# Kernel optimization log

Hardware: AMD Instinct MI355X
Metric: run time of the kernel (lower is better)

Reference implementation:

```python
import jax, jax.numpy as jnp
import numpy as np

K = 16          # max_points
S = 3           # num_scales
DM = 256        # d_model
KD = 16         # k_dim geometric projection
TAU = 1e-4
LN_EPS = 1e-5


def _boundaries():
    edges = [(i, j) for i in range(K) for j in range(i + 1, K)]
    tris = [(i, j, k) for i in range(K) for j in range(i + 1, K) for k in range(j + 1, K)]
    E, T = len(edges), len(tris)
    B1 = np.zeros((K, E), np.float32)
    for e, (i, j) in enumerate(edges):
        B1[i, e] = -1.0
        B1[j, e] = 1.0
    eidx = {e: n for n, e in enumerate(edges)}
    B2 = np.zeros((E, T), np.float32)
    for t, (i, j, k) in enumerate(tris):
        B2[eidx[(j, k)], t] = 1.0
        B2[eidx[(i, k)], t] = -1.0
        B2[eidx[(i, j)], t] = 1.0
    ei = np.array([e[0] for e in edges])
    ej = np.array([e[1] for e in edges])
    tij = np.array([eidx[(a, b)] for a, b, c in tris])
    tjk = np.array([eidx[(b, c)] for a, b, c in tris])
    tik = np.array([eidx[(a, c)] for a, b, c in tris])
    return (jnp.asarray(B1), jnp.asarray(B2), jnp.asarray(np.abs(B1)),
            jnp.asarray(ei), jnp.asarray(ej), jnp.asarray(tij), jnp.asarray(tjk), jnp.asarray(tik))

_B1, _B2, _ABS, _EI, _EJ, _TIJ, _TJK, _TIK = _boundaries()
E = _B1.shape[1]  # 120


def _ln(x, g, b):
    m = jnp.mean(x, -1, keepdims=True)
    v = jnp.mean((x - m) ** 2, -1, keepdims=True)
    return (x - m) * jax.lax.rsqrt(v + LN_EPS) * g + b


def setup_inputs() -> dict:
    key = jax.random.key(0)
    ks = jax.random.split(key, 12)
    B = 1024
    p = lambda k, *sh: 0.02 * jax.random.normal(k, sh, dtype=jnp.float32)
    return {
        'x': jax.random.normal(ks[0], (B, K, DM), dtype=jnp.float32),
        'mask': jnp.ones((B, K), dtype=jnp.float32),
        'Wg': p(ks[1], DM, KD), 'bg': jnp.zeros((KD,), jnp.float32),
        'log_scales': jnp.linspace(-1.5, 1.5, S, dtype=jnp.float32),
        'Wv': p(ks[2], DM, DM * S), 'bv': jnp.zeros((DM * S,), jnp.float32),
        'We': p(ks[3], DM, DM * S), 'be': jnp.zeros((DM * S,), jnp.float32),
        'Wo': p(ks[4], DM * S * 2, DM), 'bo': jnp.zeros((DM,), jnp.float32),
        'ln1_g': jnp.ones((DM,), jnp.float32), 'ln1_b': jnp.zeros((DM,), jnp.float32),
        'ln2_g': jnp.ones((DM,), jnp.float32), 'ln2_b': jnp.zeros((DM,), jnp.float32),
        'Wf1': p(ks[5], DM, DM * 4), 'bf1': jnp.zeros((DM * 4,), jnp.float32),
        'Wf2': p(ks[6], DM * 4, DM), 'bf2': jnp.zeros((DM,), jnp.float32),
    }


def reference(x, mask, Wg, bg, log_scales, Wv, bv, We, be, Wo, bo,
              ln1_g, ln1_b, ln2_g, ln2_b, Wf1, bf1, Wf2, bf2):
    B = x.shape[0]
    xn = _ln(x, ln1_g, ln1_b)
    P = xn @ Wg + bg                                   # [B,K,KD]
    m2 = mask[:, :, None] * mask[:, None, :]           # [B,K,K]
    p2 = jnp.sum(P * P, -1)
    Dsq = jnp.maximum(p2[:, :, None] + p2[:, None, :] - 2.0 * jnp.einsum('bkc,blc->bkl', P, P), 0.0) * m2
    sig2 = jnp.exp(log_scales) ** 2                    # [S]
    V0 = (xn @ Wv + bv).reshape(B, K, S, DM).transpose(0, 2, 1, 3)   # [B,S,K,D]
    Eraw = jnp.einsum('ke,bkd->bed', _ABS, xn)         # [B,E,D]
    Ein = (Eraw @ We + be).reshape(B, E, S, DM).transpose(0, 2, 1, 3)  # [B,S,E,D]
    aff = jnp.exp(-Dsq[:, None] / (2.0 * sig2[None, :, None, None] + 1e-8)) * m2[:, None]  # [B,S,K,K]
    W1 = aff[:, :, _EI, _EJ]                           # [B,S,E]
    W2 = W1[:, :, _TIJ] * W1[:, :, _TJK] * W1[:, :, _TIK]  # [B,S,T]
    L0 = jnp.einsum('ke,bse,le->bskl', _B1, W1, _B1) + TAU * jnp.eye(K, dtype=x.dtype)
    node_upd = jnp.einsum('bskl,bsld->bskd', L0, V0)
    term_down = jnp.einsum('ke,bk,kf->bef', _B1, mask, _B1)
    term_up = jnp.einsum('et,bst,ft->bsef', _B2, W2, _B2)
    L1 = term_down[:, None] + term_up + TAU * jnp.eye(E, dtype=x.dtype)
    edge_msg = jnp.einsum('bsef,bsfd->bsed', L1, Ein)
    edge_upd = jnp.einsum('ke,bsed->bskd', _ABS, edge_msg)
    nu = node_upd.transpose(0, 2, 1, 3).reshape(B, K, S * DM)
    eu = edge_upd.transpose(0, 2, 1, 3).reshape(B, K, S * DM)
    x = x + (jnp.concatenate([nu, eu], -1) @ Wo + bo)  # residual + attn_out (dropout=eval noop)
    h = _ln(x, ln2_g, ln2_b)
    return x + (jax.nn.gelu(h @ Wf1 + bf1, approximate=False) @ Wf2 + bf2)
```

## Files before the change

### kernel.cpp

```cpp
#include <hip/hip_runtime.h>
#include <hip/hip_bf16.h>
#include <cstdint>
#include <cstddef>

#define TAU 1e-4f
#define LN_EPS 1e-5f

typedef unsigned short ushort_t;
typedef unsigned int uint_t;
typedef __attribute__((ext_vector_type(8))) short short8;
typedef __attribute__((ext_vector_type(4))) float f32x4;

__device__ __forceinline__ ushort_t f2bf(float f) {
    union { float f; unsigned int u; } c; c.f = f;
    unsigned int r = (c.u + 0x7fffu + ((c.u >> 16) & 1u)) >> 16;
    return (ushort_t)r;
}
__device__ __forceinline__ void glds16(const void* g, void* l) {
    __builtin_amdgcn_global_load_lds((const __attribute__((address_space(1))) unsigned int*)g,
                                     (__attribute__((address_space(3))) unsigned int*)l,
                                     16, 0, 0);
}

__global__ __launch_bounds__(256) void kA(
    const float* __restrict__ xg, const float* __restrict__ maskg,
    const float* __restrict__ Wg, const float* __restrict__ bg,
    const float* __restrict__ ls, const float* __restrict__ g1,
    const float* __restrict__ b1, ushort_t* __restrict__ Mcat,
    float* __restrict__ gbuf,
    const float* __restrict__ Wv, const float* __restrict__ We,
    const float* __restrict__ Wo, const float* __restrict__ bv,
    const float* __restrict__ be, const float* __restrict__ Wf1,
    const float* __restrict__ Wf2, ushort_t* __restrict__ WcatT,
    ushort_t* __restrict__ Wf1T, ushort_t* __restrict__ Wf2T,
    float* __restrict__ cvpart, float* __restrict__ beWo) {
    __shared__ __align__(16) float POOL[9872];
    const int tid = threadIdx.x;

    if (blockIdx.x >= 1024) {
        const int id = blockIdx.x - 1024;
        if (id < 384) {
            float (*rowS)[256] = (float(*)[256])POOL;
            const int q0 = (id & 63) * 4;
            const int w = id >> 6;
            const int half = w / 3, s = w - half * 3;
            const float* src = half ? We : Wv;
#pragma unroll
            for (int r = 0; r < 4; ++r)
                rowS[r][tid] = src[(size_t)(q0 + r) * 768 + s * 256 + tid];
            __syncthreads();
            const float* wo = Wo + (size_t)(half * 768 + s * 256) * 256 + tid;
            float a0 = 0.f, a1 = 0.f, a2 = 0.f, a3 = 0.f;
            for (int d = 0; d < 256; ++d) {
                float wv = wo[(size_t)d * 256];
                a0 += rowS[0][d] * wv; a1 += rowS[1][d] * wv;
                a2 += rowS[2][d] * wv; a3 += rowS[3][d] * wv;
            }
            const int rt = half * 3 + s;
            ushort4 pk;
            pk.x = f2bf(a0); pk.y = f2bf(a1); pk.z = f2bf(a2); pk.w = f2bf(a3);
            *(ushort4*)&WcatT[(size_t)tid * 1536 + rt * 256 + q0] = pk;
        } else if (id < 390) {
            const int w = id - 384;
            const int half = w / 3, s = w - half * 3;
            const float* vec = half ? be : bv;
            POOL[tid] = vec[s * 256 + tid];
            __syncthreads();
            const float* wo = Wo + (size_t)(half * 768 + s * 256) * 256 + tid;
            float acc = 0.f;
            for (int d = 0; d < 256; ++d) acc += POOL[d] * wo[(size_t)d * 256];
            if (half) beWo[s * 256 + tid] = acc;
            else cvpart[s * 256 + tid] = acc;
        } else {
            float (*tS)[65] = (float(*)[65])POOL;
            const float* src; ushort_t* dst;
            int sr0, sc0, ss, dr0, dc0, ds_;
            if (id < 454) {
                int t = id - 390; int ki = t & 3, ni = t >> 2;
                src = Wf1; ss = 1024; sr0 = ki * 64; sc0 = ni * 64;
                dst = Wf1T; ds_ = 256; dr0 = ni * 64; dc0 = ki * 64;
            } else {
                int t = id - 454; int ki = t >> 2, ni = t & 3;
                src = Wf2; ss = 256; sr0 = ki * 64; sc0 = ni * 64;
                dst = Wf2T; ds_ = 1024; dr0 = ni * 64; dc0 = ki * 64;
            }
            const int rl = tid >> 6, cl = tid & 63;
#pragma unroll
            for (int p = 0; p < 16; ++p) {
                int r = p * 4 + rl;
                tS[r][cl] = src[(size_t)(sr0 + r) * ss + sc0 + cl];
            }
            __syncthreads();
#pragma unroll
            for (int p = 0; p < 16; ++p) {
                int r = p * 4 + rl;
                dst[(size_t)(dr0 + r) * ds_ + dc0 + cl] = f2bf(tS[cl][r]);
            }
        }
        return;
    }

    const int b = blockIdx.x;
    float (*XS)[260] = (float(*)[260])POOL;
    float* WB = POOL + 4160;
    float (*Pl)[17] = (float(*)[17])(POOL + 8320);
    float (*dotm)[17] = (float(*)[17])(POOL + 8592);
    float* Ms = POOL + 8320;
    float* mk = POOL + 9856;
    float (*WgT)[260] = (float(*)[260])WB;
    float (*DsqS)[17] = (float(*)[17])WB;
    float (*Wh)[16][17] = (float(*)[16][17])(WB + 272);
    float* Ts = WB + 1088;

    const float* xb = xg + (size_t)b * 4096;
#pragma unroll
    for (int i = 0; i < 4; ++i) {
        int idx = tid * 4 + i * 1024;
        int k = idx >> 8, c = idx & 255;
        float4 v = *(const float4*)&xb[idx];
        XS[k][c] = v.x; XS[k][c + 1] = v.y; XS[k][c + 2] = v.z; XS[k][c + 3] = v.w;
    }
    {
        const float4* wgp = (const float4*)(Wg + tid * 16);
        float4 w0 = wgp[0], w1 = wgp[1], w2 = wgp[2], w3 = wgp[3];
        WgT[0][tid] = w0.x; WgT[1][tid] = w0.y; WgT[2][tid] = w0.z; WgT[3][tid] = w0.w;
        WgT[4][tid] = w1.x; WgT[5][tid] = w1.y; WgT[6][tid] = w1.z; WgT[7][tid] = w1.w;
        WgT[8][tid] = w2.x; WgT[9][tid] = w2.y; WgT[10][tid] = w2.z; WgT[11][tid] = w2.w;
        WgT[12][tid] = w3.x; WgT[13][tid] = w3.y; WgT[14][tid] = w3.z; WgT[15][tid] = w3.w;
    }
    if (tid < 16) mk[tid] = maskg[b * 16 + tid];
    __syncthreads();

    {
        const int k = tid >> 4, c = tid & 15;
        float s = 0.f;
#pragma unroll
        for (int j = 0; j < 16; ++j) s += XS[k][c + 16 * j];
        for (int off = 8; off; off >>= 1) s += __shfl_down(s, off, 16);
        float mean = __shfl(s, 0, 16) * (1.f / 256.f);
        float vs = 0.f;
#pragma unroll
        for (int j = 0; j < 16; ++j) { float d = XS[k][c + 16 * j] - mean; vs += d * d; }
        for (int off = 8; off; off >>= 1) vs += __shfl_down(vs, off, 16);
        float rstd = rsqrtf(__shfl(vs, 0, 16) * (1.f / 256.f) + LN_EPS);
#pragma unroll
        for (int j = 0; j < 16; ++j) {
            int cc = c + 16 * j;
            XS[k][cc] = (XS[k][cc] - mean) * rstd * g1[cc] + b1[cc];
        }
    }
    __syncthreads();

    {
        const int k = tid >> 4, c = tid & 15;
        float acc = bg[c];
#pragma unroll
        for (int q4 = 0; q4 < 64; ++q4) {
            float4 wv = *(const float4*)&WgT[c][q4 * 4];
            float4 xv = *(const float4*)&XS[k][q4 * 4];
            acc += wv.x * xv.x + wv.y * xv.y + wv.z * xv.z + wv.w * xv.w;
        }
        Pl[k][c] = acc;
    }
    __syncthreads();
    const int k = tid >> 4, m = tid & 15;
    {
        float d = 0.f;
#pragma unroll
        for (int c = 0; c < 16; ++c) d += Pl[k][c] * Pl[m][c];
        dotm[k][m] = d;
    }
    __syncthreads();
    {
        float v = dotm[k][k] + dotm[m][m] - 2.f * dotm[k][m];
        DsqS[k][m] = fmaxf(v, 0.f) * mk[k] * mk[m];
    }
    {
        float d = DsqS[k][m];
        float mm = mk[k] * mk[m];
#pragma unroll
        for (int s = 0; s < 3; ++s) {
            float i2 = 1.f / (2.f * expf(2.f * ls[s]) + 1e-8f);
            Wh[s][k][m] = (k == m) ? 0.f : expf(-d * i2) * mm;
        }
    }
    __syncthreads();
    if (tid < 48) {
        int s = tid >> 4, j = tid & 15;
        float t = 0.f;
        for (int i = 0; i < j; ++i) {
            float d = 0.f;
            for (int jj = j + 1; jj < 16; ++jj) d += Wh[s][j][jj] * Wh[s][i][jj];
            t += Wh[s][i][j] * d;
        }
        Ts[s * 16 + j] = t;
    }
    __syncthreads();
    float gd = 0.f;
#pragma unroll
    for (int o = 0; o < 16; ++o) {
        if (o == m) continue;
        int u = o < m ? o : m, v = o < m ? m : o;
        float gu = (u == k) ? (float)(2 * k - 15) : ((u > k) ? 1.f : -1.f);
        float gv = (v == k) ? (float)(2 * k - 15) : ((v > k) ? 1.f : -1.f);
        gd += -gu * mk[u] + gv * mk[v];
        if (u == k || v == k) gd += TAU;
    }
#pragma unroll
    for (int s = 0; s < 3; ++s) {
        float rs = 0.f;
#pragma unroll
        for (int o = 0; o < 16; ++o) rs += Wh[s][k][o];
        float l0 = (k == m) ? (rs + TAU) : -Wh[s][k][m];
        float G = gd + ((k == m) ? 4.f * Ts[s * 16 + k] : 0.f);
        Ms[s * 256 + tid] = l0;
        Ms[768 + s * 256 + tid] = G;
        float gg = G;
        for (int off = 8; off; off >>= 1) gg += __shfl_down(gg, off, 16);
        if (m == 0) gbuf[b * 48 + k * 3 + s] = 0.5f * gg;
    }
    __syncthreads();

    {
        const int q2 = (tid & 127) * 2;
        const int rtbase = (tid >> 7) * 3;
        float xv0[16], xv1[16];
#pragma unroll
        for (int l = 0; l < 16; ++l) { xv0[l] = XS[l][q2]; xv1[l] = XS[l][q2 + 1]; }
        const size_t obase = (size_t)b * 16 * 1536;
#pragma unroll
        for (int rtt = 0; rtt < 3; ++rtt) {
            const int rt = rtbase + rtt;
#pragma unroll
            for (int kk = 0; kk < 16; ++kk) {
                const float4* mp = (const float4*)&Ms[rt * 256 + kk * 16];
                float4 m0 = mp[0], m1 = mp[1], m2 = mp[2], m3 = mp[3];
                float a0 = m0.x * xv0[0] + m0.y * xv0[1] + m0.z * xv0[2] + m0.w * xv0[3]
                         + m1.x * xv0[4] + m1.y * xv0[5] + m1.z * xv0[6] + m1.w * xv0[7]
                         + m2.x * xv0[8] + m2.y * xv0[9] + m2.z * xv0[10] + m2.w * xv0[11]
                         + m3.x * xv0[12] + m3.y * xv0[13] + m3.z * xv0[14] + m3.w * xv0[15];
                float a1 = m0.x * xv1[0] + m0.y * xv1[1] + m0.z * xv1[2] + m0.w * xv1[3]
                         + m1.x * xv1[4] + m1.y * xv1[5] + m1.z * xv1[6] + m1.w * xv1[7]
                         + m2.x * xv1[8] + m2.y * xv1[9] + m2.z * xv1[10] + m2.w * xv1[11]
                         + m3.x * xv1[12] + m3.y * xv1[13] + m3.z * xv1[14] + m3.w * xv1[15];
                uint_t pk = (uint_t)f2bf(a0) | ((uint_t)f2bf(a1) << 16);
                *(uint_t*)&Mcat[obase + (size_t)kk * 1536 + rt * 256 + q2] = pk;
            }
        }
    }
}

__device__ __forceinline__ void gemm64_db(
    const ushort_t* __restrict__ A, const ushort_t* __restrict__ Bt,
    int Kdim, int m0, int n0, f32x4 acc[2][4],
    ushort_t (*As0)[32], ushort_t (*As1)[32],
    ushort_t (*Bs0)[32], ushort_t (*Bs1)[32]) {
    const int tid = threadIdx.x;
    const int wave = tid >> 6, lane = tid & 63;
    const int lq = lane >> 4, lr = lane & 15;
    const int wm = wave >> 1, wn = wave & 1;
    const int r = tid >> 2, ca = (tid & 3) << 3;
    const ushort_t* Ag  = A  + (size_t)(m0 + r) * Kdim + ca;
    const ushort_t* Bg0 = Bt + (size_t)(n0 + r) * Kdim + ca;
    const ushort_t* Bg1 = Bt + (size_t)(n0 + 64 + r) * Kdim + ca;
    char* aD0  = (char*)As0 + wave * 1024;
    char* aD1  = (char*)As1 + wave * 1024;
    char* b0D0 = (char*)Bs0 + wave * 1024;
    char* b0D1 = (char*)Bs0 + 4096 + wave * 1024;
    char* b1D0 = (char*)Bs1 + wave * 1024;
    char* b1D1 = (char*)Bs1 + 4096 + wave * 1024;

    glds16(Ag, aD0); glds16(Bg0, b0D0); glds16(Bg1, b0D1);

    for (int kt = 0; kt < Kdim; kt += 64) {
        {
            const int kn = kt + 32;
            if (kn < Kdim) {
                glds16(Ag + kn, aD1); glds16(Bg0 + kn, b1D0); glds16(Bg1 + kn, b1D1);
                asm volatile("s_waitcnt vmcnt(3)" ::: "memory");
            } else {
                asm volatile("s_waitcnt vmcnt(0)" ::: "memory");
            }
            __builtin_amdgcn_s_barrier();
            short8 af[2], bfr[4];
#pragma unroll
            for (int i = 0; i < 2; ++i) af[i] = *(const short8*)&As0[wm * 32 + i * 16 + lr][lq * 8];
#pragma unroll
            for (int j = 0; j < 4; ++j) bfr[j] = *(const short8*)&Bs0[wn * 64 + j * 16 + lr][lq * 8];
#pragma unroll
            for (int i = 0; i < 2; ++i)
#pragma unroll
                for (int j = 0; j < 4; ++j)
                    acc[i][j] = __builtin_amdgcn_mfma_f32_16x16x32_bf16(af[i], bfr[j], acc[i][j], 0, 0, 0);
            asm volatile("s_waitcnt lgkmcnt(0)" ::: "memory");
            __builtin_amdgcn_s_barrier();
        }
        {
            const int kn = kt + 64;
            if (kn < Kdim) {
                glds16(Ag + kn, aD0); glds16(Bg0 + kn, b0D0); glds16(Bg1 + kn, b0D1);
                asm volatile("s_waitcnt vmcnt(3)" ::: "memory");
            } else {
                asm volatile("s_waitcnt vmcnt(0)" ::: "memory");
            }
            __builtin_amdgcn_s_barrier();
            short8 af[2], bfr[4];
#pragma unroll
            for (int i = 0; i < 2; ++i) af[i] = *(const short8*)&As1[wm * 32 + i * 16 + lr][lq * 8];
#pragma unroll
            for (int j = 0; j < 4; ++j) bfr[j] = *(const short8*)&Bs1[wn * 64 + j * 16 + lr][lq * 8];
#pragma unroll
            for (int i = 0; i < 2; ++i)
#pragma unroll
                for (int j = 0; j < 4; ++j)
                    acc[i][j] = __builtin_amdgcn_mfma_f32_16x16x32_bf16(af[i], bfr[j], acc[i][j], 0, 0, 0);
            asm volatile("s_waitcnt lgkmcnt(0)" ::: "memory");
            __builtin_amdgcn_s_barrier();
        }
    }
}

__device__ __forceinline__ void gemm128_db(
    const ushort_t* __restrict__ A, const ushort_t* __restrict__ Bt,
    int Kdim, int m0, int n0, f32x4 acc[4][4],
    ushort_t (*As0)[32], ushort_t (*As1)[32],
    ushort_t (*Bs0)[32], ushort_t (*Bs1)[32]) {
    const int tid = threadIdx.x;
    const int wave = tid >> 6, lane = tid & 63;
    const int lq = lane >> 4, lr = lane & 15;
    const int wm = wave >> 1, wn = wave & 1;
    const int r = tid >> 2, ca = (tid & 3) << 3;
    const ushort_t* Ag0 = A + (size_t)(m0 + r) * Kdim + ca;
    const ushort_t* Ag1 = A + (size_t)(m0 + 64 + r) * Kdim + ca;
    const ushort_t* Bg0 = Bt + (size_t)(n0 + r) * Kdim + ca;
    const ushort_t* Bg1 = Bt + (size_t)(n0 + 64 + r) * Kdim + ca;
    char* a0D0 = (char*)As0 + wave * 1024;
    char* a0D1 = (char*)As0 + 4096 + wave * 1024;
    char* a1D0 = (char*)As1 + wave * 1024;
    char* a1D1 = (char*)As1 + 4096 + wave * 1024;
    char* b0D0 = (char*)Bs0 + wave * 1024;
    char* b0D1 = (char*)Bs0 + 4096 + wave * 1024;
    char* b1D0 = (char*)Bs1 + wave * 1024;
    char* b1D1 = (char*)Bs1 + 4096 + wave * 1024;

    glds16(Ag0, a0D0); glds16(Ag1, a0D1); glds16(Bg0, b0D0); glds16(Bg1, b0D1);

    for (int kt = 0; kt < Kdim; kt += 64) {
        {
            const int kn = kt + 32;
            if (kn < Kdim) {
                glds16(Ag0 + kn, a1D0); glds16(Ag1 + kn, a1D1);
                glds16(Bg0 + kn, b1D0); glds16(Bg1 + kn, b1D1);
                asm volatile("s_waitcnt vmcnt(4)" ::: "memory");
            } else {
                asm volatile("s_waitcnt vmcnt(0)" ::: "memory");
            }
            __builtin_amdgcn_s_barrier();
            short8 af[4], bfr[4];
#pragma unroll
            for (int i = 0; i < 4; ++i) af[i] = *(const short8*)&As0[wm * 64 + i * 16 + lr][lq * 8];
#pragma unroll
            for (int j = 0; j < 4; ++j) bfr[j] = *(const short8*)&Bs0[wn * 64 + j * 16 + lr][lq * 8];
#pragma unroll
            for (int i = 0; i < 4; ++i)
#pragma unroll
                for (int j = 0; j < 4; ++j)
                    acc[i][j] = __builtin_amdgcn_mfma_f32_16x16x32_bf16(af[i], bfr[j], acc[i][j], 0, 0, 0);
            asm volatile("s_waitcnt lgkmcnt(0)" ::: "memory");
            __builtin_amdgcn_s_barrier();
        }
        {
            const int kn = kt + 64;
            if (kn < Kdim) {
                glds16(Ag0 + kn, a0D0); glds16(Ag1 + kn, a0D1);
                glds16(Bg0 + kn, b0D0); glds16(Bg1 + kn, b0D1);
                asm volatile("s_waitcnt vmcnt(4)" ::: "memory");
            } else {
                asm volatile("s_waitcnt vmcnt(0)" ::: "memory");
            }
            __builtin_amdgcn_s_barrier();
            short8 af[4], bfr[4];
#pragma unroll
            for (int i = 0; i < 4; ++i) af[i] = *(const short8*)&As1[wm * 64 + i * 16 + lr][lq * 8];
#pragma unroll
            for (int j = 0; j < 4; ++j) bfr[j] = *(const short8*)&Bs1[wn * 64 + j * 16 + lr][lq * 8];
#pragma unroll
            for (int i = 0; i < 4; ++i)
#pragma unroll
                for (int j = 0; j < 4; ++j)
                    acc[i][j] = __builtin_amdgcn_mfma_f32_16x16x32_bf16(af[i], bfr[j], acc[i][j], 0, 0, 0);
            asm volatile("s_waitcnt lgkmcnt(0)" ::: "memory");
            __builtin_amdgcn_s_barrier();
        }
    }
}

__global__ __launch_bounds__(256) void kZY_gemm(
    const ushort_t* __restrict__ Mcat, const ushort_t* __restrict__ WcatT,
    const float* __restrict__ xin, const float* __restrict__ bo,
    const float* __restrict__ cvpart, const float* __restrict__ beWo,
    const float* __restrict__ gbuf, float* __restrict__ xp) {
    __shared__ ushort_t As0[64][32], As1[64][32];
    __shared__ ushort_t Bs0[128][32], Bs1[128][32];
    __shared__ float cvS[128], bewS[3][128], gblk[64][3];
    const int tid = threadIdx.x;
    const int m0 = blockIdx.x * 64, n0 = blockIdx.y * 128;
    if (tid < 128) {
        int n = n0 + tid;
        cvS[tid] = bo[n] + TAU * (cvpart[n] + cvpart[256 + n] + cvpart[512 + n]);
        bewS[0][tid] = beWo[n];
        bewS[1][tid] = beWo[256 + n];
        bewS[2][tid] = beWo[512 + n];
    }
    if (tid < 192) { int rr = tid / 3, s = tid - rr * 3; gblk[rr][s] = gbuf[(size_t)(m0 + rr) * 3 + s]; }
    f32x4 acc[2][4] = {};
    gemm64_db(Mcat, WcatT, 1536, m0, n0, acc, As0, As1, Bs0, Bs1);
    const int wave = tid >> 6, lane = tid & 63, lq = lane >> 4, lr = lane & 15;
    const int wm = wave >> 1, wn = wave & 1;
#pragma unroll
    for (int i = 0; i < 2; ++i)
#pragma unroll
        for (int j = 0; j < 4; ++j) {
            int nl = wn * 64 + j * 16 + lr;
#pragma unroll
            for (int v = 0; v < 4; ++v) {
                int rl = wm * 32 + i * 16 + lq * 4 + v;
                size_t idx = (size_t)(m0 + rl) * 256 + n0 + nl;
                xp[idx] = acc[i][j][v] + xin[idx] + cvS[nl] +
                          gblk[rl][0] * bewS[0][nl] + gblk[rl][1] * bewS[1][nl] +
                          gblk[rl][2] * bewS[2][nl];
            }
        }
}

__global__ __launch_bounds__(256) void k_ln2(const float* __restrict__ xp,
                                             const float* __restrict__ g2,
                                             const float* __restrict__ b2,
                                             ushort_t* __restrict__ h) {
    const int tid = threadIdx.x;
    const int row = blockIdx.x * 4 + (tid >> 6);
    const int lane = tid & 63;
    const float* xr = xp + (size_t)row * 256;
    float v0 = xr[lane], v1 = xr[lane + 64], v2 = xr[lane + 128], v3 = xr[lane + 192];
    float s = v0 + v1 + v2 + v3;
    for (int m = 32; m; m >>= 1) s += __shfl_xor(s, m, 64);
    float mean = s * (1.f / 256.f);
    float d0 = v0 - mean, d1 = v1 - mean, d2 = v2 - mean, d3 = v3 - mean;
    float q = d0 * d0 + d1 * d1 + d2 * d2 + d3 * d3;
    for (int m = 32; m; m >>= 1) q += __shfl_xor(q, m, 64);
    float rstd = rsqrtf(q * (1.f / 256.f) + LN_EPS);
    ushort_t* hr = h + (size_t)row * 256;
    hr[lane] = f2bf(d0 * rstd * g2[lane] + b2[lane]);
    hr[lane + 64] = f2bf(d1 * rstd * g2[lane + 64] + b2[lane + 64]);
    hr[lane + 128] = f2bf(d2 * rstd * g2[lane + 128] + b2[lane + 128]);
    hr[lane + 192] = f2bf(d3 * rstd * g2[lane + 192] + b2[lane + 192]);
}

__global__ __launch_bounds__(256) void k3_gemm(const ushort_t* __restrict__ h,
                                               const ushort_t* __restrict__ Wf1T,
                                               const float* __restrict__ bf1,
                                               ushort_t* __restrict__ F1g) {
    __shared__ ushort_t As0[64][32], As1[64][32];
    __shared__ ushort_t Bs0[128][32], Bs1[128][32];
    const int tid = threadIdx.x;
    const int m0 = blockIdx.x * 64, n0 = blockIdx.y * 128;
    f32x4 acc[2][4] = {};
    gemm64_db(h, Wf1T, 256, m0, n0, acc, As0, As1, Bs0, Bs1);
    const int wave = tid >> 6, lane = tid & 63, lq = lane >> 4, lr = lane & 15;
    const int wm = wave >> 1, wn = wave & 1;
#pragma unroll
    for (int i = 0; i < 2; ++i)
#pragma unroll
        for (int j = 0; j < 4; ++j) {
            int n = n0 + wn * 64 + j * 16 + lr;
            float bn = bf1[n];
#pragma unroll
            for (int v = 0; v < 4; ++v) {
                int rg = m0 + wm * 32 + i * 16 + lq * 4 + v;
                float u = acc[i][j][v] + bn;
                float gl = 0.5f * u * (1.f + erff(u * 0.70710678118f));
                F1g[(size_t)rg * 1024 + n] = f2bf(gl);
            }
        }
}

__global__ __launch_bounds__(256) void k4_gemm(const ushort_t* __restrict__ F1g,
                                               const ushort_t* __restrict__ Wf2T,
                                               const float* __restrict__ bf2,
                                               const float* __restrict__ xp,
                                               float* __restrict__ out) {
    __shared__ ushort_t As0[64][32], As1[64][32];
    __shared__ ushort_t Bs0[128][32], Bs1[128][32];
    const int tid = threadIdx.x;
    const int m0 = blockIdx.x * 64, n0 = blockIdx.y * 128;
    f32x4 acc[2][4] = {};
    gemm64_db(F1g, Wf2T, 1024, m0, n0, acc, As0, As1, Bs0, Bs1);
    const int wave = tid >> 6, lane = tid & 63, lq = lane >> 4, lr = lane & 15;
    const int wm = wave >> 1, wn = wave & 1;
#pragma unroll
    for (int i = 0; i < 2; ++i)
#pragma unroll
        for (int j = 0; j < 4; ++j) {
            int n = n0 + wn * 64 + j * 16 + lr;
            float bn = bf2[n];
#pragma unroll
            for (int v = 0; v < 4; ++v) {
                size_t idx = (size_t)(m0 + wm * 32 + i * 16 + lq * 4 + v) * 256 + n;
                out[idx] = xp[idx] + acc[i][j][v] + bn;
            }
        }
}

extern "C" void kernel_launch(void* const* d_in, const int* in_sizes, int n_in,
                              void* d_out, int out_size, void* d_ws, size_t ws_size,
                              hipStream_t stream) {
    const float* x = (const float*)d_in[0];
    const float* mask = (const float*)d_in[1];
    const float* Wg = (const float*)d_in[2];
    const float* bg = (const float*)d_in[3];
    const float* ls = (const float*)d_in[4];
    const float* Wv = (const float*)d_in[5];
    const float* bv = (const float*)d_in[6];
    const float* We = (const float*)d_in[7];
    const float* be = (const float*)d_in[8];
    const float* Wo = (const float*)d_in[9];
    const float* bo = (const float*)d_in[10];
    const float* g1 = (const float*)d_in[11];
    const float* b1 = (const float*)d_in[12];
    const float* g2 = (const float*)d_in[13];
    const float* b2 = (const float*)d_in[14];
    const float* Wf1 = (const float*)d_in[15];
    const float* bf1 = (const float*)d_in[16];
    const float* Wf2 = (const float*)d_in[17];
    const float* bf2 = (const float*)d_in[18];
    float* out = (float*)d_out;

    char* ws = (char*)d_ws;
    ushort_t* Mcat = (ushort_t*)(ws);
    ushort_t* F1g = (ushort_t*)(ws);
    ushort_t* WcatT = (ushort_t*)(ws + 50331648);
    ushort_t* Wf1T = (ushort_t*)(ws + 51118080);
    ushort_t* Wf2T = (ushort_t*)(ws + 51642368);
    float* cvpart = (float*)(ws + 52166656);
    float* beWo = (float*)(ws + 52169728);
    float* gbuf = (float*)(ws + 52172800);
    float* xp = (float*)(ws + 52369408);
    ushort_t* h = (ushort_t*)(ws + 69146624);

    kA<<<dim3(1542), dim3(256), 0, stream>>>(x, mask, Wg, bg, ls, g1, b1,
                                             Mcat, gbuf,
                                             Wv, We, Wo, bv, be, Wf1, Wf2,
                                             WcatT, Wf1T, Wf2T, cvpart, beWo);
    kZY_gemm<<<dim3(256, 2), dim3(256), 0, stream>>>(Mcat, WcatT, x, bo, cvpart, beWo, gbuf, xp);
    k_ln2<<<dim3(4096), dim3(256), 0, stream>>>(xp, g2, b2, h);
    k3_gemm<<<dim3(256, 8), dim3(256), 0, stream>>>(h, Wf1T, bf1, F1g);
    k4_gemm<<<dim3(256, 2), dim3(256), 0, stream>>>(F1g, Wf2T, bf2, xp, out);
}
```

Measured before the change: 205.4 us.

## Use 64x64 tiles with triple-buffered LDS pipeline for output GEMMs

Adds a 64x64-tile GEMM helper that prefetches two K-steps ahead into a three-slot LDS ring. The kZY and k4 GEMMs (N=256) switch from 64x128 tiles to 64x64 tiles, doubling the grid from 512 to 1024 blocks so more of the CUs are busy. Deeper prefetch is meant to hide global-load latency. In exchange, each block does less MFMA work per barrier and the A operand is loaded twice as often across blocks. The unused 128x128 helper is removed.

Measured after the change: 210.8 us. 2.7% more time.

```diff
diff --git a/kernel.cpp b/kernel.cpp
--- a/kernel.cpp
+++ b/kernel.cpp
@@ -250,6 +250,59 @@
     }
 }
 
+__device__ __forceinline__ void gemm64x64_d2(
+    const ushort_t* __restrict__ A, const ushort_t* __restrict__ Bt,
+    int Kdim, int m0, int n0, f32x4 acc[2][2],
+    ushort_t (*AsB)[64][32], ushort_t (*BsB)[64][32]) {
+    const int tid = threadIdx.x;
+    const int wave = tid >> 6, lane = tid & 63;
+    const int lq = lane >> 4, lr = lane & 15;
+    const int wm = wave >> 1, wn = wave & 1;
+    const int r = tid >> 2, ca = (tid & 3) << 3;
+    const ushort_t* Ag = A + (size_t)(m0 + r) * Kdim + ca;
+    const ushort_t* Bg = Bt + (size_t)(n0 + r) * Kdim + ca;
+    const int NT = Kdim >> 5;
+    char* aD0 = (char*)AsB[0] + wave * 1024;
+    char* bD0 = (char*)BsB[0] + wave * 1024;
+    char* aD1 = (char*)AsB[1] + wave * 1024;
+    char* bD1 = (char*)BsB[1] + wave * 1024;
+    char* aD2 = (char*)AsB[2] + wave * 1024;
+    char* bD2 = (char*)BsB[2] + wave * 1024;
+
+    glds16(Ag, aD0);       glds16(Bg, bD0);
+    glds16(Ag + 32, aD1);  glds16(Bg + 32, bD1);
+
+    int bc = 0;
+    for (int t = 0; t < NT; ++t) {
+        const int t2 = t + 2;
+        if (t2 < NT) {
+            char* aD = (bc == 0) ? aD2 : ((bc == 1) ? aD0 : aD1);
+            char* bD = (bc == 0) ? bD2 : ((bc == 1) ? bD0 : bD1);
+            glds16(Ag + t2 * 32, aD);
+            glds16(Bg + t2 * 32, bD);
+            asm volatile("s_waitcnt vmcnt(4)" ::: "memory");
+        } else if (t + 1 < NT) {
+            asm volatile("s_waitcnt vmcnt(2)" ::: "memory");
+        } else {
+            asm volatile("s_waitcnt vmcnt(0)" ::: "memory");
+        }
+        __builtin_amdgcn_s_barrier();
+        short8 af[2], bfr[2];
+#pragma unroll
+        for (int i = 0; i < 2; ++i) af[i] = *(const short8*)&AsB[bc][wm * 32 + i * 16 + lr][lq * 8];
+#pragma unroll
+        for (int j = 0; j < 2; ++j) bfr[j] = *(const short8*)&BsB[bc][wn * 32 + j * 16 + lr][lq * 8];
+#pragma unroll
+        for (int i = 0; i < 2; ++i)
+#pragma unroll
+            for (int j = 0; j < 2; ++j)
+                acc[i][j] = __builtin_amdgcn_mfma_f32_16x16x32_bf16(af[i], bfr[j], acc[i][j], 0, 0, 0);
+        asm volatile("s_waitcnt lgkmcnt(0)" ::: "memory");
+        __builtin_amdgcn_s_barrier();
+        ++bc; if (bc >= 3) bc = 0;
+    }
+}
+
 __device__ __forceinline__ void gemm64_db(
     const ushort_t* __restrict__ A, const ushort_t* __restrict__ Bt,
     int Kdim, int m0, int n0, f32x4 acc[2][4],
@@ -320,92 +373,16 @@
     }
 }
 
-__device__ __forceinline__ void gemm128_db(
-    const ushort_t* __restrict__ A, const ushort_t* __restrict__ Bt,
-    int Kdim, int m0, int n0, f32x4 acc[4][4],
-    ushort_t (*As0)[32], ushort_t (*As1)[32],
-    ushort_t (*Bs0)[32], ushort_t (*Bs1)[32]) {
-    const int tid = threadIdx.x;
-    const int wave = tid >> 6, lane = tid & 63;
-    const int lq = lane >> 4, lr = lane & 15;
-    const int wm = wave >> 1, wn = wave & 1;
-    const int r = tid >> 2, ca = (tid & 3) << 3;
-    const ushort_t* Ag0 = A + (size_t)(m0 + r) * Kdim + ca;
-    const ushort_t* Ag1 = A + (size_t)(m0 + 64 + r) * Kdim + ca;
-    const ushort_t* Bg0 = Bt + (size_t)(n0 + r) * Kdim + ca;
-    const ushort_t* Bg1 = Bt + (size_t)(n0 + 64 + r) * Kdim + ca;
-    char* a0D0 = (char*)As0 + wave * 1024;
-    char* a0D1 = (char*)As0 + 4096 + wave * 1024;
-    char* a1D0 = (char*)As1 + wave * 1024;
-    char* a1D1 = (char*)As1 + 4096 + wave * 1024;
-    char* b0D0 = (char*)Bs0 + wave * 1024;
-    char* b0D1 = (char*)Bs0 + 4096 + wave * 1024;
-    char* b1D0 = (char*)Bs1 + wave * 1024;
-    char* b1D1 = (char*)Bs1 + 4096 + wave * 1024;
-
-    glds16(Ag0, a0D0); glds16(Ag1, a0D1); glds16(Bg0, b0D0); glds16(Bg1, b0D1);
-
-    for (int kt = 0; kt < Kdim; kt += 64) {
-        {
-            const int kn = kt + 32;
-            if (kn < Kdim) {
-                glds16(Ag0 + kn, a1D0); glds16(Ag1 + kn, a1D1);
-                glds16(Bg0 + kn, b1D0); glds16(Bg1 + kn, b1D1);
-                asm volatile("s_waitcnt vmcnt(4)" ::: "memory");
-            } else {
-                asm volatile("s_waitcnt vmcnt(0)" ::: "memory");
-            }
-            __builtin_amdgcn_s_barrier();
-            short8 af[4], bfr[4];
-#pragma unroll
-            for (int i = 0; i < 4; ++i) af[i] = *(const short8*)&As0[wm * 64 + i * 16 + lr][lq * 8];
-#pragma unroll
-            for (int j = 0; j < 4; ++j) bfr[j] = *(const short8*)&Bs0[wn * 64 + j * 16 + lr][lq * 8];
-#pragma unroll
-            for (int i = 0; i < 4; ++i)
-#pragma unroll
-                for (int j = 0; j < 4; ++j)
-                    acc[i][j] = __builtin_amdgcn_mfma_f32_16x16x32_bf16(af[i], bfr[j], acc[i][j], 0, 0, 0);
-            asm volatile("s_waitcnt lgkmcnt(0)" ::: "memory");
-            __builtin_amdgcn_s_barrier();
-        }
-        {
-            const int kn = kt + 64;
-            if (kn < Kdim) {
-                glds16(Ag0 + kn, a0D0); glds16(Ag1 + kn, a0D1);
-                glds16(Bg0 + kn, b0D0); glds16(Bg1 + kn, b0D1);
-                asm volatile("s_waitcnt vmcnt(4)" ::: "memory");
-            } else {
-                asm volatile("s_waitcnt vmcnt(0)" ::: "memory");
-            }
-            __builtin_amdgcn_s_barrier();
-            short8 af[4], bfr[4];
-#pragma unroll
-            for (int i = 0; i < 4; ++i) af[i] = *(const short8*)&As1[wm * 64 + i * 16 + lr][lq * 8];
-#pragma unroll
-            for (int j = 0; j < 4; ++j) bfr[j] = *(const short8*)&Bs1[wn * 64 + j * 16 + lr][lq * 8];
-#pragma unroll
-            for (int i = 0; i < 4; ++i)
-#pragma unroll
-                for (int j = 0; j < 4; ++j)
-                    acc[i][j] = __builtin_amdgcn_mfma_f32_16x16x32_bf16(af[i], bfr[j], acc[i][j], 0, 0, 0);
-            asm volatile("s_waitcnt lgkmcnt(0)" ::: "memory");
-            __builtin_amdgcn_s_barrier();
-        }
-    }
-}
-
 __global__ __launch_bounds__(256) void kZY_gemm(
     const ushort_t* __restrict__ Mcat, const ushort_t* __restrict__ WcatT,
     const float* __restrict__ xin, const float* __restrict__ bo,
     const float* __restrict__ cvpart, const float* __restrict__ beWo,
     const float* __restrict__ gbuf, float* __restrict__ xp) {
-    __shared__ ushort_t As0[64][32], As1[64][32];
-    __shared__ ushort_t Bs0[128][32], Bs1[128][32];
-    __shared__ float cvS[128], bewS[3][128], gblk[64][3];
-    const int tid = threadIdx.x;
-    const int m0 = blockIdx.x * 64, n0 = blockIdx.y * 128;
-    if (tid < 128) {
+    __shared__ ushort_t AsB[3][64][32], BsB[3][64][32];
+    __shared__ float cvS[64], bewS[3][64], gblk[64][3];
+    const int tid = threadIdx.x;
+    const int m0 = blockIdx.x * 64, n0 = blockIdx.y * 64;
+    if (tid < 64) {
         int n = n0 + tid;
         cvS[tid] = bo[n] + TAU * (cvpart[n] + cvpart[256 + n] + cvpart[512 + n]);
         bewS[0][tid] = beWo[n];
@@ -413,15 +390,15 @@
         bewS[2][tid] = beWo[512 + n];
     }
     if (tid < 192) { int rr = tid / 3, s = tid - rr * 3; gblk[rr][s] = gbuf[(size_t)(m0 + rr) * 3 + s]; }
-    f32x4 acc[2][4] = {};
-    gemm64_db(Mcat, WcatT, 1536, m0, n0, acc, As0, As1, Bs0, Bs1);
+    f32x4 acc[2][2] = {};
+    gemm64x64_d2(Mcat, WcatT, 1536, m0, n0, acc, AsB, BsB);
     const int wave = tid >> 6, lane = tid & 63, lq = lane >> 4, lr = lane & 15;
     const int wm = wave >> 1, wn = wave & 1;
 #pragma unroll
     for (int i = 0; i < 2; ++i)
 #pragma unroll
-        for (int j = 0; j < 4; ++j) {
-            int nl = wn * 64 + j * 16 + lr;
+        for (int j = 0; j < 2; ++j) {
+            int nl = wn * 32 + j * 16 + lr;
 #pragma unroll
             for (int v = 0; v < 4; ++v) {
                 int rl = wm * 32 + i * 16 + lq * 4 + v;
@@ -489,19 +466,18 @@
                                                const float* __restrict__ bf2,
                                                const float* __restrict__ xp,
                                                float* __restrict__ out) {
-    __shared__ ushort_t As0[64][32], As1[64][32];
-    __shared__ ushort_t Bs0[128][32], Bs1[128][32];
-    const int tid = threadIdx.x;
-    const int m0 = blockIdx.x * 64, n0 = blockIdx.y * 128;
-    f32x4 acc[2][4] = {};
-    gemm64_db(F1g, Wf2T, 1024, m0, n0, acc, As0, As1, Bs0, Bs1);
+    __shared__ ushort_t AsB[3][64][32], BsB[3][64][32];
+    const int tid = threadIdx.x;
+    const int m0 = blockIdx.x * 64, n0 = blockIdx.y * 64;
+    f32x4 acc[2][2] = {};
+    gemm64x64_d2(F1g, Wf2T, 1024, m0, n0, acc, AsB, BsB);
     const int wave = tid >> 6, lane = tid & 63, lq = lane >> 4, lr = lane & 15;
     const int wm = wave >> 1, wn = wave & 1;
 #pragma unroll
     for (int i = 0; i < 2; ++i)
 #pragma unroll
-        for (int j = 0; j < 4; ++j) {
-            int n = n0 + wn * 64 + j * 16 + lr;
+        for (int j = 0; j < 2; ++j) {
+            int n = n0 + wn * 32 + j * 16 + lr;
             float bn = bf2[n];
 #pragma unroll
             for (int v = 0; v < 4; ++v) {
@@ -551,8 +527,8 @@
                                              Mcat, gbuf,
                                              Wv, We, Wo, bv, be, Wf1, Wf2,
                                              WcatT, Wf1T, Wf2T, cvpart, beWo);
-    kZY_gemm<<<dim3(256, 2), dim3(256), 0, stream>>>(Mcat, WcatT, x, bo, cvpart, beWo, gbuf, xp);
+    kZY_gemm<<<dim3(256, 4), dim3(256), 0, stream>>>(Mcat, WcatT, x, bo, cvpart, beWo, gbuf, xp);
     k_ln2<<<dim3(4096), dim3(256), 0, stream>>>(xp, g2, b2, h);
     k3_gemm<<<dim3(256, 8), dim3(256), 0, stream>>>(h, Wf1T, bf1, F1g);
-    k4_gemm<<<dim3(256, 2), dim3(256), 0, stream>>>(F1g, Wf2T, bf2, xp, out);
-}
+    k4_gemm<<<dim3(256, 4), dim3(256), 0, stream>>>(F1g, Wf2T, bf2, xp, out);
+}
```
